# Kernel optimization log

Hardware: AMD Instinct MI355X
Metric: run time of the kernel (lower is better)

Reference implementation:

```python
import jax, jax.numpy as jnp
import numpy as np

B = 2048          # number of graphs
NPG = 128         # nodes per graph (hard-coded by lin1 = Linear(128*hid, 1))
N = B * NPG       # total nodes = 262144
DEG = 16          # avg degree
EPG = NPG * DEG   # edges per graph
E = B * EPG       # total edges = 4194304
IN_CH = 151
HID = 64


def setup_inputs() -> dict:
    key = jax.random.key(0)
    ks = jax.random.split(key, 6)
    x = jax.random.normal(ks[0], (N, IN_CH), jnp.float32)
    # within-graph random edges: local index in [0, NPG) plus per-graph node offset
    src_loc = jax.random.randint(ks[1], (E,), 0, NPG, dtype=jnp.int32)
    dst_loc = jax.random.randint(ks[2], (E,), 0, NPG, dtype=jnp.int32)
    off = ((jnp.arange(E, dtype=jnp.int32) // EPG) * NPG)
    edge_index = jnp.stack([src_loc + off, dst_loc + off])  # [2, E] int32
    edge_weight = jax.random.uniform(ks[3], (E,), jnp.float32)
    batch = jnp.arange(N, dtype=jnp.int32) // NPG  # sorted graph ids
    W1 = jax.random.normal(ks[4], (IN_CH, HID), jnp.float32) / np.sqrt(IN_CH)
    b1 = jnp.zeros((HID,), jnp.float32)
    Wlin = jax.random.normal(ks[5], (NPG * HID, 1), jnp.float32) / np.sqrt(NPG * HID)
    blin = jnp.zeros((1,), jnp.float32)
    return {"x": x, "edge_index": edge_index, "edge_weight": edge_weight,
            "batch": batch, "W1": W1, "b1": b1, "Wlin": Wlin, "blin": blin}


def _gcn_conv(x, row, col, w, W, b, num_nodes):
    # PyG GCNConv: h = x @ W; out[col] += dinv[row]*w*dinv[col] * h[row]; out += b
    h = x @ W                                        # [N, HID]
    deg = jax.ops.segment_sum(w, col, num_segments=num_nodes)
    dinv = jnp.where(deg > 0, jax.lax.rsqrt(deg), 0.0)
    norm = dinv[row] * w * dinv[col]                 # [E+N]
    out = jax.ops.segment_sum(h[row] * norm[:, None], col, num_segments=num_nodes)
    return out + b


def reference(x, edge_index, edge_weight, batch, W1, b1, Wlin, blin):
    num_nodes = x.shape[0]
    # add self-loops with weight 1 (GCNConv default)
    sl = jnp.arange(num_nodes, dtype=edge_index.dtype)
    row = jnp.concatenate([edge_index[0], sl])
    col = jnp.concatenate([edge_index[1], sl])
    w = jnp.concatenate([edge_weight, jnp.ones((num_nodes,), x.dtype)])
    h = jax.nn.relu(_gcn_conv(x, row, col, w, W1, b1, num_nodes))  # [N, HID]
    # linearize: nodes are batch-sorted, 128 per graph -> [B, 128*HID]
    g = h.reshape(num_nodes // NPG, NPG * h.shape[1])
    return jax.nn.sigmoid(g @ Wlin + blin)  # [B, 1]
```

## Files before the change

kernel.cpp:

```cpp
#include <hip/hip_runtime.h>
#include <math.h>

#define NPG 128
#define HID 64
#define ICH 151
#define EPG 2048
#define TPB 512
#define EPT (EPG / TPB)
#define BTS 168
#define HTS 136
#define ASS 132
#define BT_OFF 17408

typedef __attribute__((ext_vector_type(8))) short  short8;
typedef __attribute__((ext_vector_type(4))) float  floatx4;

static __device__ __forceinline__ unsigned short f2bf(float v) {
    unsigned u = __builtin_bit_cast(unsigned, v);
    return (unsigned short)((u + 0x7fffu + ((u >> 16) & 1u)) >> 16);
}
static __device__ __forceinline__ unsigned packbf(float a, float b) {
    return (unsigned)f2bf(a) | ((unsigned)f2bf(b) << 16);
}
static __device__ __forceinline__ short8 pack8(const float* v) {
    union { unsigned u[4]; short8 s; } r;
    r.u[0] = packbf(v[0], v[1]);
    r.u[1] = packbf(v[2], v[3]);
    r.u[2] = packbf(v[4], v[5]);
    r.u[3] = packbf(v[6], v[7]);
    return r.s;
}

__global__ __launch_bounds__(TPB, 6) void gcn_fused(
    const float* __restrict__ x,
    const int*   __restrict__ erow,
    const int*   __restrict__ ecol,
    const float* __restrict__ ew,
    const float* __restrict__ W1,
    const float* __restrict__ b1,
    const float* __restrict__ Wlin,
    const float* __restrict__ blin,
    float* __restrict__ out)
{
    __shared__ __align__(16) char smem[38912];
    __shared__ float deg[NPG];
    __shared__ float dinv[NPG];
    __shared__ float red[TPB / 64];

    short* ht = (short*)smem;
    short* bt = (short*)(smem + BT_OFF);
    float* As = (float*)(smem + BT_OFF);

    const int t    = threadIdx.x;
    const int g    = blockIdx.x;
    const int lane = t & 63;
    const int wv   = t >> 6;
    const int c16  = lane & 15;
    const int kq   = (lane >> 4) * 8;

    if (t < NPG) deg[t] = 1.0f;

    int   ep_[EPT];
    float nw_[EPT];
    const int ebase = g * EPG;
    #pragma unroll
    for (int it = 0; it < EPT; ++it) {
        int e = ebase + t + it * TPB;
        int rl = erow[e] & (NPG - 1);
        int cl = ecol[e] & (NPG - 1);
        ep_[it] = (cl << 7) | rl;
        nw_[it] = ew[e];
    }

    short8 af[5];
    {
        const float* xr = x + (size_t)g * (NPG * ICH) + (wv * 16 + c16) * ICH;
        #pragma unroll
        for (int s = 0; s < 5; ++s) {
            float v[8];
            #pragma unroll
            for (int j = 0; j < 8; ++j) {
                int k = s * 32 + kq + j;
                v[j] = (k < ICH) ? xr[k] : 0.0f;
            }
            af[s] = pack8(v);
        }
    }

    {
        const int c = t & 63, k0 = (t >> 6) * 2;
        for (int k = k0; k < BTS; k += 16) {
            float w0 = (k     < ICH) ? W1[k * HID + c]       : 0.0f;
            float w1 = (k + 1 < ICH) ? W1[(k + 1) * HID + c] : 0.0f;
            *(unsigned*)&bt[c * BTS + k] = packbf(w0, w1);
        }
    }
    __syncthreads();

    #pragma unroll
    for (int it = 0; it < EPT; ++it)
        atomicAdd(&deg[ep_[it] >> 7], nw_[it]);

    #pragma unroll
    for (int n = 0; n < 4; ++n) {
        floatx4 acc = {0.0f, 0.0f, 0.0f, 0.0f};
        #pragma unroll
        for (int s = 0; s < 5; ++s) {
            short8 b = *(const short8*)&bt[(n * 16 + c16) * BTS + s * 32 + kq];
            acc = __builtin_amdgcn_mfma_f32_16x16x32_bf16(af[s], b, acc, 0, 0, 0);
        }
        int col = n * 16 + c16;
        int row = wv * 16 + (lane >> 4) * 4;
        *(int2*)&ht[col * HTS + row] =
            make_int2((int)packbf(acc[0], acc[1]), (int)packbf(acc[2], acc[3]));
    }
    __syncthreads();

    if (t < NPG) dinv[t] = rsqrtf(deg[t]);
    __syncthreads();

    #pragma unroll
    for (int it = 0; it < EPT; ++it) {
        int rl = ep_[it] & (NPG - 1), cl = ep_[it] >> 7;
        nw_[it] = dinv[rl] * nw_[it] * dinv[cl];
    }

    float partial = 0.0f;
    const int mt   = wv >> 2;
    const int ntb  = wv & 3;
    const int col  = ntb * 16 + c16;
    const int arow = mt * 16 + c16;
    const float b1v = b1[col];

    for (int q = 0; q < 4; ++q) {
        for (int p = t; p < 32 * ASS / 4; p += TPB)
            ((floatx4*)As)[p] = (floatx4){0.0f, 0.0f, 0.0f, 0.0f};
        __syncthreads();

        #pragma unroll
        for (int it = 0; it < EPT; ++it) {
            int cl = ep_[it] >> 7;
            if ((cl >> 5) == q)
                atomicAdd(&As[(cl & 31) * ASS + (ep_[it] & (NPG - 1))], nw_[it]);
        }
        if (t < 32) {
            int i = q * 32 + t;
            atomicAdd(&As[t * ASS + i], dinv[i] * dinv[i]);
        }
        __syncthreads();

        short8 afr[4];
        #pragma unroll
        for (int ks = 0; ks < 4; ++ks) {
            const float* ap = &As[arow * ASS + ks * 32 + kq];
            floatx4 a0 = *(const floatx4*)ap;
            floatx4 a1 = *(const floatx4*)(ap + 4);
            float v[8] = {a0[0], a0[1], a0[2], a0[3], a1[0], a1[1], a1[2], a1[3]};
            afr[ks] = pack8(v);
        }
        __syncthreads();
        floatx4 acc = {0.0f, 0.0f, 0.0f, 0.0f};
        #pragma unroll
        for (int ks = 0; ks < 4; ++ks) {
            short8 b = *(const short8*)&ht[col * HTS + ks * 32 + kq];
            acc = __builtin_amdgcn_mfma_f32_16x16x32_bf16(afr[ks], b, acc, 0, 0, 0);
        }
        int node0 = q * 32 + mt * 16 + (lane >> 4) * 4;
        #pragma unroll
        for (int r = 0; r < 4; ++r) {
            float v = fmaxf(acc[r] + b1v, 0.0f);
            partial += v * Wlin[(node0 + r) * HID + col];
        }
    }

    #pragma unroll
    for (int o = 32; o > 0; o >>= 1)
        partial += __shfl_down(partial, o, 64);
    if (lane == 0) red[wv] = partial;
    __syncthreads();
    if (t == 0) {
        float tot = blin[0];
        #pragma unroll
        for (int i = 0; i < TPB / 64; ++i) tot += red[i];
        out[g] = 1.0f / (1.0f + expf(-tot));
    }
}

extern "C" void kernel_launch(void* const* d_in, const int* in_sizes, int n_in,
                              void* d_out, int out_size, void* d_ws, size_t ws_size,
                              hipStream_t stream) {
    const float* x    = (const float*)d_in[0];
    const int*   ei   = (const int*)d_in[1];
    const float* ew   = (const float*)d_in[2];
    const float* W1   = (const float*)d_in[4];
    const float* b1   = (const float*)d_in[5];
    const float* Wlin = (const float*)d_in[6];
    const float* blin = (const float*)d_in[7];
    float* out = (float*)d_out;

    const int E = in_sizes[1] / 2;
    const int B = out_size;

    gcn_fused<<<B, TPB, 0, stream>>>(x, ei, ei + E, ew, W1, b1, Wlin, blin, out);
}
```

Measured before the change: 90.93 us.

## Precompute bf16 transposed W1 in prep kernel and aggregate adjacency in two halves

Result: faster. 83.66 us (-8.0%).

```diff
diff --git a/kernel.cpp b/kernel.cpp
--- a/kernel.cpp
+++ b/kernel.cpp
@@ -7,10 +7,10 @@
 #define EPG 2048
 #define TPB 512
 #define EPT (EPG / TPB)
-#define BTS 168
+#define KP  160
 #define HTS 136
 #define ASS 132
-#define BT_OFF 17408
+#define AS_OFF 17408
 
 typedef __attribute__((ext_vector_type(8))) short  short8;
 typedef __attribute__((ext_vector_type(4))) float  floatx4;
@@ -31,25 +31,33 @@
     return r.s;
 }
 
+__global__ __launch_bounds__(512) void gcn_prep(const float* __restrict__ W1,
+                                                short* __restrict__ W1T) {
+    int i = threadIdx.x + blockIdx.x * 512;
+    if (i < HID * KP) {
+        int ch = i / KP, k = i - ch * KP;
+        W1T[i] = (short)f2bf((k < ICH) ? W1[k * HID + ch] : 0.0f);
+    }
+}
+
 __global__ __launch_bounds__(TPB, 6) void gcn_fused(
     const float* __restrict__ x,
     const int*   __restrict__ erow,
     const int*   __restrict__ ecol,
     const float* __restrict__ ew,
-    const float* __restrict__ W1,
+    const short* __restrict__ W1T,
     const float* __restrict__ b1,
     const float* __restrict__ Wlin,
     const float* __restrict__ blin,
     float* __restrict__ out)
 {
-    __shared__ __align__(16) char smem[38912];
+    __shared__ __align__(16) char smem[AS_OFF + 64 * ASS * 4];
     __shared__ float deg[NPG];
     __shared__ float dinv[NPG];
     __shared__ float red[TPB / 64];
 
     short* ht = (short*)smem;
-    short* bt = (short*)(smem + BT_OFF);
-    float* As = (float*)(smem + BT_OFF);
+    float* As = (float*)(smem + AS_OFF);
 
     const int t    = threadIdx.x;
     const int g    = blockIdx.x;
@@ -86,15 +94,6 @@
             af[s] = pack8(v);
         }
     }
-
-    {
-        const int c = t & 63, k0 = (t >> 6) * 2;
-        for (int k = k0; k < BTS; k += 16) {
-            float w0 = (k     < ICH) ? W1[k * HID + c]       : 0.0f;
-            float w1 = (k + 1 < ICH) ? W1[(k + 1) * HID + c] : 0.0f;
-            *(unsigned*)&bt[c * BTS + k] = packbf(w0, w1);
-        }
-    }
     __syncthreads();
 
     #pragma unroll
@@ -106,7 +105,7 @@
         floatx4 acc = {0.0f, 0.0f, 0.0f, 0.0f};
         #pragma unroll
         for (int s = 0; s < 5; ++s) {
-            short8 b = *(const short8*)&bt[(n * 16 + c16) * BTS + s * 32 + kq];
+            short8 b = *(const short8*)&W1T[(n * 16 + c16) * KP + s * 32 + kq];
             acc = __builtin_amdgcn_mfma_f32_16x16x32_bf16(af[s], b, acc, 0, 0, 0);
         }
         int col = n * 16 + c16;
@@ -126,25 +125,21 @@
     }
 
     float partial = 0.0f;
-    const int mt   = wv >> 2;
-    const int ntb  = wv & 3;
-    const int col  = ntb * 16 + c16;
-    const int arow = mt * 16 + c16;
-    const float b1v = b1[col];
-
-    for (int q = 0; q < 4; ++q) {
-        for (int p = t; p < 32 * ASS / 4; p += TPB)
+    const int mrow = (wv >> 1) * 16 + c16;
+
+    for (int half = 0; half < 2; ++half) {
+        for (int p = t; p < 64 * ASS / 4; p += TPB)
             ((floatx4*)As)[p] = (floatx4){0.0f, 0.0f, 0.0f, 0.0f};
         __syncthreads();
 
         #pragma unroll
         for (int it = 0; it < EPT; ++it) {
             int cl = ep_[it] >> 7;
-            if ((cl >> 5) == q)
-                atomicAdd(&As[(cl & 31) * ASS + (ep_[it] & (NPG - 1))], nw_[it]);
-        }
-        if (t < 32) {
-            int i = q * 32 + t;
+            if ((cl >> 6) == half)
+                atomicAdd(&As[(cl & 63) * ASS + (ep_[it] & (NPG - 1))], nw_[it]);
+        }
+        if (t < 64) {
+            int i = half * 64 + t;
             atomicAdd(&As[t * ASS + i], dinv[i] * dinv[i]);
         }
         __syncthreads();
@@ -152,25 +147,31 @@
         short8 afr[4];
         #pragma unroll
         for (int ks = 0; ks < 4; ++ks) {
-            const float* ap = &As[arow * ASS + ks * 32 + kq];
+            const float* ap = &As[mrow * ASS + ks * 32 + kq];
             floatx4 a0 = *(const floatx4*)ap;
             floatx4 a1 = *(const floatx4*)(ap + 4);
             float v[8] = {a0[0], a0[1], a0[2], a0[3], a1[0], a1[1], a1[2], a1[3]};
             afr[ks] = pack8(v);
         }
+        #pragma unroll
+        for (int nn = 0; nn < 2; ++nn) {
+            int nt2 = (wv & 1) * 2 + nn;
+            floatx4 acc = {0.0f, 0.0f, 0.0f, 0.0f};
+            #pragma unroll
+            for (int ks = 0; ks < 4; ++ks) {
+                short8 b = *(const short8*)&ht[(nt2 * 16 + c16) * HTS + ks * 32 + kq];
+                acc = __builtin_amdgcn_mfma_f32_16x16x32_bf16(afr[ks], b, acc, 0, 0, 0);
+            }
+            int col = nt2 * 16 + c16;
+            float b1v = b1[col];
+            int node0 = half * 64 + (wv >> 1) * 16 + (lane >> 4) * 4;
+            #pragma unroll
+            for (int r = 0; r < 4; ++r) {
+                float v = fmaxf(acc[r] + b1v, 0.0f);
+                partial += v * Wlin[(node0 + r) * HID + col];
+            }
+        }
         __syncthreads();
-        floatx4 acc = {0.0f, 0.0f, 0.0f, 0.0f};
-        #pragma unroll
-        for (int ks = 0; ks < 4; ++ks) {
-            short8 b = *(const short8*)&ht[col * HTS + ks * 32 + kq];
-            acc = __builtin_amdgcn_mfma_f32_16x16x32_bf16(afr[ks], b, acc, 0, 0, 0);
-        }
-        int node0 = q * 32 + mt * 16 + (lane >> 4) * 4;
-        #pragma unroll
-        for (int r = 0; r < 4; ++r) {
-            float v = fmaxf(acc[r] + b1v, 0.0f);
-            partial += v * Wlin[(node0 + r) * HID + col];
-        }
     }
 
     #pragma unroll
@@ -201,5 +202,8 @@
     const int E = in_sizes[1] / 2;
     const int B = out_size;
 
-    gcn_fused<<<B, TPB, 0, stream>>>(x, ei, ei + E, ew, W1, b1, Wlin, blin, out);
-}
+    short* W1T = (short*)d_ws;
+
+    gcn_prep<<<(HID * KP + 511) / 512, 512, 0, stream>>>(W1, W1T);
+    gcn_fused<<<B, TPB, 0, stream>>>(x, ei, ei + E, ew, W1T, b1, Wlin, blin, out);
+}
```
